# Optimization experiments

Measured on AMD Instinct MI355X. Metric: run time of the kernel, lower is better.

## Reference

```python
import jax, jax.numpy as jnp
import numpy as np

N, T, F_IN, HEADS, FILT = 50000, 12, 128, 4, 32
D = HEADS * FILT  # 128
E = 800000
NEG_SLOPE = 0.2  # PyG GATConv default leaky_relu slope


def setup_inputs() -> dict:
    key = jax.random.key(0)
    ks = jax.random.split(key, 10)
    s = lambda k, shape, fan: (jax.random.normal(k, shape, jnp.float32) / np.float32(np.sqrt(fan)))
    x_sequence = jax.random.normal(ks[0], (N, T, F_IN), dtype=jnp.float32)
    edge_index_sequence = jax.random.randint(ks[1], (T, 2, E), 0, N, dtype=jnp.int32)
    W_gat = s(ks[2], (F_IN, D), F_IN)          # GATConv lin weight
    a_src = s(ks[3], (HEADS, FILT), FILT)      # att_src
    a_dst = s(ks[4], (HEADS, FILT), FILT)      # att_dst
    b_gat = jnp.zeros((D,), jnp.float32)
    W_ih = s(ks[5], (3 * D, D), D)             # GRU weight_ih_l0 (r,z,n)
    W_hh = s(ks[6], (3 * D, D), D)             # GRU weight_hh_l0
    b_ih = jnp.zeros((3 * D,), jnp.float32)
    b_hh = jnp.zeros((3 * D,), jnp.float32)
    W_lin = s(ks[7], (1, D), D)
    b_lin = jnp.zeros((1,), jnp.float32)
    return dict(x_sequence=x_sequence, edge_index_sequence=edge_index_sequence,
                W_gat=W_gat, a_src=a_src, a_dst=a_dst, b_gat=b_gat,
                W_ih=W_ih, W_hh=W_hh, b_ih=b_ih, b_hh=b_hh,
                W_lin=W_lin, b_lin=b_lin)


def _gat_t(x_t, src, dst, W_gat, a_src, a_dst, b_gat):
    # x_t: [N, F_IN], src/dst: [E+N] (self-loops appended, PyG default)
    h = (x_t @ W_gat).reshape(N, HEADS, FILT)          # [N, H, C]
    al_src = jnp.sum(h * a_src, axis=-1)               # [N, H]
    al_dst = jnp.sum(h * a_dst, axis=-1)               # [N, H]
    e = jax.nn.leaky_relu(al_src[src] + al_dst[dst], NEG_SLOPE)  # [Etot, H]
    m = jax.ops.segment_max(e, dst, num_segments=N)    # softmax over incoming edges per dst node
    e = jnp.exp(e - m[dst])
    denom = jax.ops.segment_sum(e, dst, num_segments=N)
    alpha = e / (denom[dst] + 1e-16)                   # [Etot, H]
    msg = h[src] * alpha[:, :, None]                   # [Etot, H, C]
    out = jax.ops.segment_sum(msg, dst, num_segments=N)
    return out.reshape(N, D) + b_gat                   # concat heads + bias


def reference(x_sequence, edge_index_sequence, W_gat, a_src, a_dst, b_gat,
              W_ih, W_hh, b_ih, b_hh, W_lin, b_lin):
    x_tnf = jnp.transpose(x_sequence, (1, 0, 2))       # [T, N, F_IN]
    loops = jnp.arange(N, dtype=edge_index_sequence.dtype)
    src = jnp.concatenate([edge_index_sequence[:, 0, :], jnp.broadcast_to(loops, (T, N))], axis=1)
    dst = jnp.concatenate([edge_index_sequence[:, 1, :], jnp.broadcast_to(loops, (T, N))], axis=1)
    gat = jax.vmap(lambda x, s, d: _gat_t(x, s, d, W_gat, a_src, a_dst, b_gat))
    g = jax.nn.relu(gat(x_tnf, src, dst))              # [T, N, D]

    def gru_step(h, x):  # torch GRU gate order: r, z, n
        gi = x @ W_ih.T + b_ih
        gh = h @ W_hh.T + b_hh
        i_r, i_z, i_n = jnp.split(gi, 3, axis=-1)
        h_r, h_z, h_n = jnp.split(gh, 3, axis=-1)
        r = jax.nn.sigmoid(i_r + h_r)
        z = jax.nn.sigmoid(i_z + h_z)
        n = jnp.tanh(i_n + r * h_n)
        return (1.0 - z) * n + z * h, None

    h0 = jnp.zeros((N, D), x_sequence.dtype)
    h_last, _ = jax.lax.scan(gru_step, h0, g)          # only last timestep output is used
    return (h_last @ W_lin.T + b_lin)[:, 0]            # [N]
```

## Files before the change

kernel.cpp:

```cpp
#include <hip/hip_runtime.h>
#include <cstddef>

#define NN 50000
#define TT 12
#define FIN 128
#define DD 128
#define HH 4
#define EE 800000
#define MTOT (NN * TT)
#define NEG 0.2f

#define BSH 6
#define NB 782
#define CAPB 1536
#define BMAX CAPB
#define EPB2 8192
#define FB2 98
#define GGRID (TT * NB)
#define GPX (GGRID / 8)

typedef __attribute__((ext_vector_type(8))) short bf16x8;
typedef __attribute__((ext_vector_type(4))) float f32x4;

__device__ __forceinline__ ushort f2b(float x) {
    unsigned int u = __builtin_bit_cast(unsigned int, x);
    unsigned int r = (u + 0x7FFFu + ((u >> 16) & 1u)) >> 16;
    return (ushort)r;
}
__device__ __forceinline__ float b2f(ushort u) {
    unsigned int v = ((unsigned int)u) << 16;
    return __builtin_bit_cast(float, v);
}

__global__ __launch_bounds__(256) void prep_wg_kernel(
    const float* __restrict__ Wg, ushort* __restrict__ Wgh, ushort* __restrict__ Wgl)
{
    int idx = blockIdx.x * 256 + threadIdx.x;
    int fi = idx >> 9, rem = idx & 511;
    int l = rem >> 3, j = rem & 7;
    int kb = fi >> 3, cf = fi & 7;
    int k = kb * 32 + (l >> 4) * 8 + j;
    int col = cf * 16 + (l & 15);
    float v = Wg[(size_t)k * DD + col];
    ushort hi = f2b(v);
    Wgh[idx] = hi;
    Wgl[idx] = f2b(v - b2f(hi));
}

__global__ __launch_bounds__(256) void gemm_all_kernel(
    const float* __restrict__ x, const ushort* __restrict__ Wgh, const ushort* __restrict__ Wgl,
    const float* __restrict__ a_src, const float* __restrict__ a_dst,
    ushort* __restrict__ hbf, float* __restrict__ alsrc, float* __restrict__ aldst)
{
    __shared__ ushort sAh[64 * 128];
    const int tid = threadIdx.x;
    const int w = tid >> 6, l = tid & 63;
    const int m0 = blockIdx.x * 64;

    #pragma unroll
    for (int i = 0; i < 8; i++) {
        int fl = tid + 256 * i;
        int row = fl >> 5, q = fl & 31;
        float4 v = *(const float4*)&x[(size_t)(m0 + row) * FIN + q * 4];
        ushort hi[4] = {f2b(v.x), f2b(v.y), f2b(v.z), f2b(v.w)};
        int byteoff = row * 256 + ((q * 8) ^ ((row & 7) << 4));
        *(uint2*)((char*)sAh + byteoff) = *(uint2*)hi;
    }
    __syncthreads();

    f32x4 acc[4][2];
    #pragma unroll
    for (int i = 0; i < 4; i++)
        #pragma unroll
        for (int s = 0; s < 2; s++) acc[i][s] = (f32x4){0.f, 0.f, 0.f, 0.f};

    const bf16x8* Bh = (const bf16x8*)Wgh;
    const bf16x8* Bl = (const bf16x8*)Wgl;
    #pragma unroll
    for (int kb = 0; kb < 4; kb++) {
        bf16x8 ah[4];
        #pragma unroll
        for (int i = 0; i < 4; i++) {
            int rl = i * 16 + (l & 15);
            int byteoff = rl * 256 + (((kb * 64) + ((l >> 4) * 16)) ^ ((rl & 7) << 4));
            ah[i] = *(const bf16x8*)((const char*)sAh + byteoff);
        }
        bf16x8 bh[2], bl[2];
        #pragma unroll
        for (int s = 0; s < 2; s++) {
            int fi = kb * 8 + 2 * w + s;
            bh[s] = Bh[(size_t)fi * 64 + l];
            bl[s] = Bl[(size_t)fi * 64 + l];
        }
        #pragma unroll
        for (int i = 0; i < 4; i++)
            #pragma unroll
            for (int s = 0; s < 2; s++) {
                acc[i][s] = __builtin_amdgcn_mfma_f32_16x16x32_bf16(ah[i], bh[s], acc[i][s], 0, 0, 0);
                acc[i][s] = __builtin_amdgcn_mfma_f32_16x16x32_bf16(ah[i], bl[s], acc[i][s], 0, 0, 0);
            }
    }

    #pragma unroll
    for (int i = 0; i < 4; i++)
        #pragma unroll
        for (int s = 0; s < 2; s++) {
            int jj = (2 * w + s) * 16 + (l & 15);
            #pragma unroll
            for (int r = 0; r < 4; r++) {
                int m = m0 + i * 16 + (l >> 4) * 4 + r;
                int n = m / TT;
                int t = m - n * TT;
                hbf[((size_t)t * NN + n) * DD + jj] = f2b(acc[i][s][r]);
            }
        }

    const float as0 = a_src[w * 32 + (l & 15)];
    const float as1 = a_src[w * 32 + 16 + (l & 15)];
    const float ad0 = a_dst[w * 32 + (l & 15)];
    const float ad1 = a_dst[w * 32 + 16 + (l & 15)];
    #pragma unroll
    for (int i = 0; i < 4; i++) {
        #pragma unroll
        for (int r = 0; r < 4; r++) {
            float p1 = acc[i][0][r] * as0 + acc[i][1][r] * as1;
            float p2 = acc[i][0][r] * ad0 + acc[i][1][r] * ad1;
            #pragma unroll
            for (int mk = 1; mk < 16; mk <<= 1) {
                p1 += __shfl_xor(p1, mk);
                p2 += __shfl_xor(p2, mk);
            }
            if ((l & 15) == 0) {
                int m = m0 + i * 16 + (l >> 4) * 4 + r;
                int n = m / TT;
                int t = m - n * TT;
                size_t base = ((size_t)t * NN + n) * 4 + w;
                alsrc[base] = p1;
                aldst[base] = p2;
            }
        }
    }
}

__global__ __launch_bounds__(256) void init_cur_kernel(int* __restrict__ cur)
{
    int i = blockIdx.x * 256 + threadIdx.x;
    if (i < TT * NB) cur[i] = i * CAPB;
}

__global__ __launch_bounds__(512) void fill2_kernel(
    const int* __restrict__ ei, int* __restrict__ cur, uint* __restrict__ bbuf)
{
    __shared__ int hcnt[NB];
    __shared__ int hbase[NB];
    const int t = blockIdx.x / FB2;
    const int blk = blockIdx.x - t * FB2;
    const int tid = threadIdx.x;
    const int* srcp = ei + (size_t)t * 2 * EE;
    const int* dstp = srcp + EE;

    for (int b = tid; b < NB; b += 512) hcnt[b] = 0;
    __syncthreads();

    const int ebase = blk * EPB2;
    uint vals[16];
    #pragma unroll
    for (int k = 0; k < 16; k++) {
        int e = ebase + k * 512 + tid;
        uint v = 0xffffffffu;
        if (e < EE) {
            int s = srcp[e];
            int d = dstp[e];
            v = ((uint)d << 16) | (uint)s;
            atomicAdd(&hcnt[d >> BSH], 1);
        }
        vals[k] = v;
    }
    __syncthreads();
    for (int b = tid; b < NB; b += 512) {
        int c = hcnt[b];
        if (c > 0) hbase[b] = atomicAdd(&cur[t * NB + b], c);
        hcnt[b] = 0;
    }
    __syncthreads();
    #pragma unroll
    for (int k = 0; k < 16; k++) {
        uint v = vals[k];
        if (v != 0xffffffffu) {
            int b = v >> 22;
            int r = atomicAdd(&hcnt[b], 1);
            bbuf[hbase[b] + r] = v;
        }
    }
}

__global__ __launch_bounds__(512) void gather_all_kernel(
    const int* __restrict__ cur, const uint* __restrict__ bbuf,
    const float* __restrict__ alsrc_a, const float* __restrict__ aldst_a,
    const uint* __restrict__ hbf32_a, const float* __restrict__ bgat,
    uint* __restrict__ Ag_a)
{
    __shared__ uint ent[BMAX];
    __shared__ ushort ssrc[BMAX];
    __shared__ int h64[64];
    __shared__ int p64[65];
    __shared__ int cur64[64];
    const int bid = blockIdx.x;
    const int swz = (bid & 7) * GPX + (bid >> 3);
    const int t = swz / NB;
    const int bkt = swz - t * NB;
    const int ci = t * NB + bkt;
    const int tid = threadIdx.x;
    const int dbase = bkt << BSH;

    const float* alsrc = alsrc_a + (size_t)t * NN * HH;
    const float* aldst = aldst_a + (size_t)t * NN * HH;
    const uint* hbf32 = hbf32_a + (size_t)t * NN * 64;
    uint* Ag = Ag_a + (size_t)t * NN * 64;

    const int lo0 = ci * CAPB;
    int cnt = cur[ci] - lo0;
    if (cnt > BMAX) cnt = BMAX;

    if (tid < 64) h64[tid] = 0;
    __syncthreads();
    for (int i = tid; i < cnt; i += 512) {
        uint e = bbuf[lo0 + i];
        ent[i] = e;
        atomicAdd(&h64[(e >> 16) & 63], 1);
    }
    __syncthreads();
    if (tid < 64) {
        int v = h64[tid];
        #pragma unroll
        for (int off = 1; off < 64; off <<= 1) {
            int u = __shfl_up(v, off);
            if (tid >= off) v += u;
        }
        p64[tid + 1] = v;
        if (tid == 0) p64[0] = 0;
        cur64[tid] = v - h64[tid];
    }
    __syncthreads();
    for (int i = tid; i < cnt; i += 512) {
        uint e = ent[i];
        int pos = atomicAdd(&cur64[(e >> 16) & 63], 1);
        ssrc[pos] = (ushort)(e & 0xffffu);
    }
    __syncthreads();

    const int w = tid >> 6, lane = tid & 63, hd = lane >> 4;
    const float bg0 = bgat[2 * lane], bg1 = bgat[2 * lane + 1];
    for (int q = 0; q < 8; q++) {
        int nd = w * 8 + q;
        int d = dbase + nd;
        if (d >= NN) break;
        float adh = aldst[(size_t)d * 4 + hd];
        float a = alsrc[(size_t)d * 4 + hd] + adh;
        a = fmaxf(a, NEG * a);
        float wt = __expf(a);
        float den = wt;
        uint hw = hbf32[(size_t)d * 64 + lane];
        float acc0 = __builtin_bit_cast(float, hw << 16) * wt;
        float acc1 = __builtin_bit_cast(float, hw & 0xffff0000u) * wt;
        const int e1 = p64[nd + 1];
        #pragma unroll 2
        for (int e = p64[nd]; e < e1; e++) {
            int s = ssrc[e];
            float aa = alsrc[(size_t)s * 4 + hd] + adh;
            aa = fmaxf(aa, NEG * aa);
            float wgt = __expf(aa);
            uint hh = hbf32[(size_t)s * 64 + lane];
            acc0 += __builtin_bit_cast(float, hh << 16) * wgt;
            acc1 += __builtin_bit_cast(float, hh & 0xffff0000u) * wgt;
            den += wgt;
        }
        float invd = 1.f / (den + 1e-16f);
        float g0 = fmaxf(acc0 * invd + bg0, 0.f);
        float g1 = fmaxf(acc1 * invd + bg1, 0.f);
        Ag[(size_t)d * 64 + lane] = (uint)f2b(g0) | ((uint)f2b(g1) << 16);
    }
}

__global__ __launch_bounds__(256) void prep_b_kernel(
    const float* __restrict__ Wih, const float* __restrict__ Whh, ushort* __restrict__ Bswz)
{
    int idx = blockIdx.x * 256 + threadIdx.x;
    int fi = idx >> 9;
    int rem = idx & 511;
    int l = rem >> 3, j = rem & 7;
    int kb = fi >> 5, c = fi & 31;
    int g = c >> 3, cf = c & 7;
    int k = kb * 32 + (l >> 4) * 8 + j;
    int jj = cf * 16 + (l & 15);
    float v;
    if (g == 0)      v = (k < 128) ? Wih[(size_t)jj * DD + k]         : Whh[(size_t)jj * DD + k - 128];
    else if (g == 1) v = (k < 128) ? Wih[(size_t)(128 + jj) * DD + k] : Whh[(size_t)(128 + jj) * DD + k - 128];
    else if (g == 2) v = (k < 128) ? Wih[(size_t)(256 + jj) * DD + k] : 0.f;
    else             v = (k < 128) ? 0.f : Whh[(size_t)(256 + jj) * DD + k - 128];
    Bswz[idx] = f2b(v);
}

__global__ __launch_bounds__(256, 2) void gru_mfma_kernel(
    const uint* __restrict__ Agp, const ushort* __restrict__ Bswz,
    float* __restrict__ hstate, const float* __restrict__ bih, const float* __restrict__ bhh,
    const float* __restrict__ wl, const float* __restrict__ bl,
    float* __restrict__ out, int last)
{
    __shared__ ushort sA[64 * 256];
    __shared__ float outacc[64];
    const int tid = threadIdx.x;
    const int w = tid >> 6, l = tid & 63;
    const int n0 = blockIdx.x * 64;

    if (tid < 64) outacc[tid] = 0.f;
    #pragma unroll
    for (int i = 0; i < 4; i++) {
        int flat = tid + 256 * i;
        int row = flat >> 4, gc = flat & 15;
        int n = n0 + row;
        uint4 vg = make_uint4(0u, 0u, 0u, 0u);
        ushort hv[8] = {0, 0, 0, 0, 0, 0, 0, 0};
        if (n < NN) {
            vg = *(const uint4*)&Agp[(size_t)n * 64 + gc * 4];
            float4 ha = *(const float4*)&hstate[(size_t)n * DD + gc * 8];
            float4 hb = *(const float4*)&hstate[(size_t)n * DD + gc * 8 + 4];
            hv[0] = f2b(ha.x); hv[1] = f2b(ha.y); hv[2] = f2b(ha.z); hv[3] = f2b(ha.w);
            hv[4] = f2b(hb.x); hv[5] = f2b(hb.y); hv[6] = f2b(hb.z); hv[7] = f2b(hb.w);
        }
        int sw = (row & 7) << 4;
        *(uint4*)((char*)sA + row * 512 + ((gc * 16) ^ sw)) = vg;
        *(uint4*)((char*)sA + row * 512 + ((256 + gc * 16) ^ sw)) = *(uint4*)hv;
    }
    __syncthreads();

    f32x4 acc[4][4][2];
    #pragma unroll
    for (int i = 0; i < 4; i++)
        #pragma unroll
        for (int g = 0; g < 4; g++)
            #pragma unroll
            for (int s = 0; s < 2; s++)
                acc[i][g][s] = (f32x4){0.f, 0.f, 0.f, 0.f};

    const bf16x8* Bf = (const bf16x8*)Bswz;
    #pragma unroll
    for (int kb = 0; kb < 8; kb++) {
        bf16x8 a[4];
        #pragma unroll
        for (int i = 0; i < 4; i++) {
            int rl = i * 16 + (l & 15);
            int byteoff = rl * 512 + (((kb * 64) + ((l >> 4) * 16)) ^ ((rl & 7) << 4));
            a[i] = *(const bf16x8*)((const char*)sA + byteoff);
        }
        bf16x8 b[4][2];
        #pragma unroll
        for (int g = 0; g < 4; g++)
            #pragma unroll
            for (int s = 0; s < 2; s++)
                b[g][s] = Bf[(size_t)(kb * 32 + g * 8 + 2 * w + s) * 64 + l];
        #pragma unroll
        for (int i = 0; i < 4; i++)
            #pragma unroll
            for (int g = 0; g < 4; g++)
                #pragma unroll
                for (int s = 0; s < 2; s++)
                    acc[i][g][s] = __builtin_amdgcn_mfma_f32_16x16x32_bf16(
                        a[i], b[g][s], acc[i][g][s], 0, 0, 0);
    }

    #pragma unroll
    for (int s = 0; s < 2; s++) {
        int jj = (2 * w + s) * 16 + (l & 15);
        float br  = bih[jj] + bhh[jj];
        float bz  = bih[128 + jj] + bhh[128 + jj];
        float bin = bih[256 + jj];
        float bhn = bhh[256 + jj];
        float wlc = wl[jj];
        #pragma unroll
        for (int i = 0; i < 4; i++) {
            #pragma unroll
            for (int r = 0; r < 4; r++) {
                int row = i * 16 + (l >> 4) * 4 + r;
                int n = n0 + row;
                if (n >= NN) continue;
                float rp = acc[i][0][s][r] + br;
                float zp = acc[i][1][s][r] + bz;
                float rg = 1.f / (1.f + __expf(-rp));
                float zg = 1.f / (1.f + __expf(-zp));
                float nv = tanhf(acc[i][2][s][r] + bin + rg * (acc[i][3][s][r] + bhn));
                float hold = hstate[(size_t)n * DD + jj];
                float hnew = (1.f - zg) * nv + zg * hold;
                if (!last) hstate[(size_t)n * DD + jj] = hnew;
                else atomicAdd(&outacc[row], hnew * wlc);
            }
        }
    }
    if (last) {
        __syncthreads();
        int n = n0 + tid;
        if (tid < 64 && n < NN) out[n] = outacc[tid] + bl[0];
    }
}

extern "C" void kernel_launch(void* const* d_in, const int* in_sizes, int n_in,
                              void* d_out, int out_size, void* d_ws, size_t ws_size,
                              hipStream_t stream)
{
    const float* x     = (const float*)d_in[0];
    const int*   ei    = (const int*)d_in[1];
    const float* Wg    = (const float*)d_in[2];
    const float* a_src = (const float*)d_in[3];
    const float* a_dst = (const float*)d_in[4];
    const float* b_gat = (const float*)d_in[5];
    const float* Wih   = (const float*)d_in[6];
    const float* Whh   = (const float*)d_in[7];
    const float* bih   = (const float*)d_in[8];
    const float* bhh   = (const float*)d_in[9];
    const float* Wl    = (const float*)d_in[10];
    const float* bl    = (const float*)d_in[11];
    float* out = (float*)d_out;

    char* ws = (char*)d_ws;
    float* hstate  = (float*)ws;                                  ws += (size_t)NN * DD * 4;
    float* alsrc   = (float*)ws;                                  ws += (size_t)MTOT * HH * 4;
    float* aldst   = (float*)ws;                                  ws += (size_t)MTOT * HH * 4;
    uint* Agall    = (uint*)ws;                                   ws += (size_t)MTOT * 64 * 4;
    ushort* Bswz   = (ushort*)ws;                                 ws += 131072 * 2;
    ushort* Wgh    = (ushort*)ws;                                 ws += 16384 * 2;
    ushort* Wgl    = (ushort*)ws;                                 ws += 16384 * 2;
    ushort* hbf    = (ushort*)ws;                                 ws += (size_t)MTOT * DD * 2;
    int* cur       = (int*)ws;                                    ws += (size_t)TT * NB * 4;
    uint* bbuf     = (uint*)ws;                                   ws += (size_t)TT * NB * CAPB * 4;

    hipMemsetAsync(hstate, 0, (size_t)NN * DD * sizeof(float), stream);

    init_cur_kernel<<<(TT * NB + 255) / 256, 256, 0, stream>>>(cur);
    prep_b_kernel<<<512, 256, 0, stream>>>(Wih, Whh, Bswz);
    prep_wg_kernel<<<64, 256, 0, stream>>>(Wg, Wgh, Wgl);

    gemm_all_kernel<<<MTOT / 64, 256, 0, stream>>>(x, Wgh, Wgl, a_src, a_dst, hbf, alsrc, aldst);

    fill2_kernel<<<TT * FB2, 512, 0, stream>>>(ei, cur, bbuf);
    gather_all_kernel<<<GGRID, 512, 0, stream>>>(
        cur, bbuf, alsrc, aldst, (const uint*)hbf, b_gat, Agall);

    for (int t = 0; t < TT; t++) {
        gru_mfma_kernel<<<(NN + 63) / 64, 256, 0, stream>>>(
            Agall + (size_t)t * NN * 64, Bswz, hstate, bih, bhh, Wl, bl, out, t == TT - 1);
    }
}
```

Baseline: 1.179 ms.

## Fuse three GRU timesteps per launch, keep bf16 hidden state in LDS

The GRU kernel now runs three timesteps per launch, so there are four launches instead of twelve. The hidden state stays in shared memory as bf16 between steps and is written to global memory (as bf16 instead of fp32) only after the third step. This cuts global hidden-state traffic and launch count. It also raises the gather loop unroll from 2 to 4. The hidden state is now carried in bf16 across steps, which adds some rounding error compared with the fp32 hstate before.

```diff
diff --git a/kernel.cpp b/kernel.cpp
--- a/kernel.cpp
+++ b/kernel.cpp
@@ -264,7 +264,7 @@
         float acc0 = __builtin_bit_cast(float, hw << 16) * wt;
         float acc1 = __builtin_bit_cast(float, hw & 0xffff0000u) * wt;
         const int e1 = p64[nd + 1];
-        #pragma unroll 2
+        #pragma unroll 4
         for (int e = p64[nd]; e < e1; e++) {
             int s = ssrc[e];
             float aa = alsrc[(size_t)s * 4 + hd] + adh;
@@ -302,10 +302,11 @@
 }
 
 __global__ __launch_bounds__(256, 2) void gru_mfma_kernel(
-    const uint* __restrict__ Agp, const ushort* __restrict__ Bswz,
-    float* __restrict__ hstate, const float* __restrict__ bih, const float* __restrict__ bhh,
+    const uint* __restrict__ Agall, int tbase,
+    uint* __restrict__ Ah, const ushort* __restrict__ Bswz,
+    const float* __restrict__ bih, const float* __restrict__ bhh,
     const float* __restrict__ wl, const float* __restrict__ bl,
-    float* __restrict__ out, int last)
+    float* __restrict__ out)
 {
     __shared__ ushort sA[64 * 256];
     __shared__ float outacc[64];
@@ -319,84 +320,110 @@
         int flat = tid + 256 * i;
         int row = flat >> 4, gc = flat & 15;
         int n = n0 + row;
-        uint4 vg = make_uint4(0u, 0u, 0u, 0u);
-        ushort hv[8] = {0, 0, 0, 0, 0, 0, 0, 0};
-        if (n < NN) {
-            vg = *(const uint4*)&Agp[(size_t)n * 64 + gc * 4];
-            float4 ha = *(const float4*)&hstate[(size_t)n * DD + gc * 8];
-            float4 hb = *(const float4*)&hstate[(size_t)n * DD + gc * 8 + 4];
-            hv[0] = f2b(ha.x); hv[1] = f2b(ha.y); hv[2] = f2b(ha.z); hv[3] = f2b(ha.w);
-            hv[4] = f2b(hb.x); hv[5] = f2b(hb.y); hv[6] = f2b(hb.z); hv[7] = f2b(hb.w);
-        }
+        uint4 vh = make_uint4(0u, 0u, 0u, 0u);
+        if (n < NN) vh = *(const uint4*)&Ah[(size_t)n * 64 + gc * 4];
         int sw = (row & 7) << 4;
-        *(uint4*)((char*)sA + row * 512 + ((gc * 16) ^ sw)) = vg;
-        *(uint4*)((char*)sA + row * 512 + ((256 + gc * 16) ^ sw)) = *(uint4*)hv;
-    }
-    __syncthreads();
-
-    f32x4 acc[4][4][2];
-    #pragma unroll
-    for (int i = 0; i < 4; i++)
-        #pragma unroll
-        for (int g = 0; g < 4; g++)
-            #pragma unroll
-            for (int s = 0; s < 2; s++)
-                acc[i][g][s] = (f32x4){0.f, 0.f, 0.f, 0.f};
+        *(uint4*)((char*)sA + row * 512 + ((256 + gc * 16) ^ sw)) = vh;
+    }
+
+    const int jjA[2] = { (2 * w) * 16 + (l & 15), (2 * w + 1) * 16 + (l & 15) };
+    float brc[2], bzc[2], binc[2], bhnc[2], wlc[2];
+    #pragma unroll
+    for (int s = 0; s < 2; s++) {
+        brc[s]  = bih[jjA[s]] + bhh[jjA[s]];
+        bzc[s]  = bih[128 + jjA[s]] + bhh[128 + jjA[s]];
+        binc[s] = bih[256 + jjA[s]];
+        bhnc[s] = bhh[256 + jjA[s]];
+        wlc[s]  = wl[jjA[s]];
+    }
 
     const bf16x8* Bf = (const bf16x8*)Bswz;
-    #pragma unroll
-    for (int kb = 0; kb < 8; kb++) {
-        bf16x8 a[4];
+
+    #pragma unroll 1
+    for (int tt = 0; tt < 3; tt++) {
+        const int t = tbase + tt;
+        const uint* Agp = Agall + (size_t)t * NN * 64;
         #pragma unroll
         for (int i = 0; i < 4; i++) {
-            int rl = i * 16 + (l & 15);
-            int byteoff = rl * 512 + (((kb * 64) + ((l >> 4) * 16)) ^ ((rl & 7) << 4));
-            a[i] = *(const bf16x8*)((const char*)sA + byteoff);
-        }
-        bf16x8 b[4][2];
-        #pragma unroll
-        for (int g = 0; g < 4; g++)
-            #pragma unroll
-            for (int s = 0; s < 2; s++)
-                b[g][s] = Bf[(size_t)(kb * 32 + g * 8 + 2 * w + s) * 64 + l];
+            int flat = tid + 256 * i;
+            int row = flat >> 4, gc = flat & 15;
+            int n = n0 + row;
+            uint4 vg = make_uint4(0u, 0u, 0u, 0u);
+            if (n < NN) vg = *(const uint4*)&Agp[(size_t)n * 64 + gc * 4];
+            int sw = (row & 7) << 4;
+            *(uint4*)((char*)sA + row * 512 + ((gc * 16) ^ sw)) = vg;
+        }
+        __syncthreads();
+
+        f32x4 acc[4][4][2];
         #pragma unroll
         for (int i = 0; i < 4; i++)
             #pragma unroll
             for (int g = 0; g < 4; g++)
                 #pragma unroll
                 for (int s = 0; s < 2; s++)
-                    acc[i][g][s] = __builtin_amdgcn_mfma_f32_16x16x32_bf16(
-                        a[i], b[g][s], acc[i][g][s], 0, 0, 0);
-    }
-
-    #pragma unroll
-    for (int s = 0; s < 2; s++) {
-        int jj = (2 * w + s) * 16 + (l & 15);
-        float br  = bih[jj] + bhh[jj];
-        float bz  = bih[128 + jj] + bhh[128 + jj];
-        float bin = bih[256 + jj];
-        float bhn = bhh[256 + jj];
-        float wlc = wl[jj];
-        #pragma unroll
-        for (int i = 0; i < 4; i++) {
-            #pragma unroll
-            for (int r = 0; r < 4; r++) {
-                int row = i * 16 + (l >> 4) * 4 + r;
-                int n = n0 + row;
-                if (n >= NN) continue;
-                float rp = acc[i][0][s][r] + br;
-                float zp = acc[i][1][s][r] + bz;
-                float rg = 1.f / (1.f + __expf(-rp));
-                float zg = 1.f / (1.f + __expf(-zp));
-                float nv = tanhf(acc[i][2][s][r] + bin + rg * (acc[i][3][s][r] + bhn));
-                float hold = hstate[(size_t)n * DD + jj];
-                float hnew = (1.f - zg) * nv + zg * hold;
-                if (!last) hstate[(size_t)n * DD + jj] = hnew;
-                else atomicAdd(&outacc[row], hnew * wlc);
-            }
-        }
-    }
-    if (last) {
+                    acc[i][g][s] = (f32x4){0.f, 0.f, 0.f, 0.f};
+
+        #pragma unroll
+        for (int kb = 0; kb < 8; kb++) {
+            bf16x8 a[4];
+            #pragma unroll
+            for (int i = 0; i < 4; i++) {
+                int rl = i * 16 + (l & 15);
+                int byteoff = rl * 512 + (((kb * 64) + ((l >> 4) * 16)) ^ ((rl & 7) << 4));
+                a[i] = *(const bf16x8*)((const char*)sA + byteoff);
+            }
+            bf16x8 b[4][2];
+            #pragma unroll
+            for (int g = 0; g < 4; g++)
+                #pragma unroll
+                for (int s = 0; s < 2; s++)
+                    b[g][s] = Bf[(size_t)(kb * 32 + g * 8 + 2 * w + s) * 64 + l];
+            #pragma unroll
+            for (int i = 0; i < 4; i++)
+                #pragma unroll
+                for (int g = 0; g < 4; g++)
+                    #pragma unroll
+                    for (int s = 0; s < 2; s++)
+                        acc[i][g][s] = __builtin_amdgcn_mfma_f32_16x16x32_bf16(
+                            a[i], b[g][s], acc[i][g][s], 0, 0, 0);
+        }
+        __syncthreads();
+
+        const bool lastT = (t == TT - 1);
+        #pragma unroll
+        for (int s = 0; s < 2; s++) {
+            const int jj = jjA[s];
+            const int hc = 16 + (jj >> 3);
+            const int hb = (jj & 7) * 2;
+            #pragma unroll
+            for (int i = 0; i < 4; i++) {
+                #pragma unroll
+                for (int r = 0; r < 4; r++) {
+                    int row = i * 16 + (l >> 4) * 4 + r;
+                    int n = n0 + row;
+                    if (n >= NN) continue;
+                    int hoff = row * 512 + ((hc * 16) ^ ((row & 7) << 4)) + hb;
+                    float hold = b2f(*(const ushort*)((const char*)sA + hoff));
+                    float rp = acc[i][0][s][r] + brc[s];
+                    float zp = acc[i][1][s][r] + bzc[s];
+                    float rg = 1.f / (1.f + __expf(-rp));
+                    float zg = 1.f / (1.f + __expf(-zp));
+                    float nv = tanhf(acc[i][2][s][r] + binc[s] + rg * (acc[i][3][s][r] + bhnc[s]));
+                    float hnew = (1.f - zg) * nv + zg * hold;
+                    if (lastT) {
+                        atomicAdd(&outacc[row], hnew * wlc[s]);
+                    } else {
+                        ushort hb16 = f2b(hnew);
+                        *(ushort*)((char*)sA + hoff) = hb16;
+                        if (tt == 2) ((ushort*)Ah)[(size_t)n * 128 + jj] = hb16;
+                    }
+                }
+            }
+        }
+    }
+
+    if (tbase + 2 == TT - 1) {
         __syncthreads();
         int n = n0 + tid;
         if (tid < 64 && n < NN) out[n] = outacc[tid] + bl[0];
@@ -422,10 +449,10 @@
     float* out = (float*)d_out;
 
     char* ws = (char*)d_ws;
-    float* hstate  = (float*)ws;                                  ws += (size_t)NN * DD * 4;
     float* alsrc   = (float*)ws;                                  ws += (size_t)MTOT * HH * 4;
     float* aldst   = (float*)ws;                                  ws += (size_t)MTOT * HH * 4;
     uint* Agall    = (uint*)ws;                                   ws += (size_t)MTOT * 64 * 4;
+    uint* Ah       = (uint*)ws;                                   ws += (size_t)NN * 64 * 4;
     ushort* Bswz   = (ushort*)ws;                                 ws += 131072 * 2;
     ushort* Wgh    = (ushort*)ws;                                 ws += 16384 * 2;
     ushort* Wgl    = (ushort*)ws;                                 ws += 16384 * 2;
@@ -433,7 +460,7 @@
     int* cur       = (int*)ws;                                    ws += (size_t)TT * NB * 4;
     uint* bbuf     = (uint*)ws;                                   ws += (size_t)TT * NB * CAPB * 4;
 
-    hipMemsetAsync(hstate, 0, (size_t)NN * DD * sizeof(float), stream);
+    hipMemsetAsync(Ah, 0, (size_t)NN * 64 * sizeof(uint), stream);
 
     init_cur_kernel<<<(TT * NB + 255) / 256, 256, 0, stream>>>(cur);
     prep_b_kernel<<<512, 256, 0, stream>>>(Wih, Whh, Bswz);
@@ -445,8 +472,8 @@
     gather_all_kernel<<<GGRID, 512, 0, stream>>>(
         cur, bbuf, alsrc, aldst, (const uint*)hbf, b_gat, Agall);
 
-    for (int t = 0; t < TT; t++) {
+    for (int tb = 0; tb < TT; tb += 3) {
         gru_mfma_kernel<<<(NN + 63) / 64, 256, 0, stream>>>(
-            Agall + (size_t)t * NN * 64, Bswz, hstate, bih, bhh, Wl, bl, out, t == TT - 1);
-    }
-}
+            Agall, tb, Ah, Bswz, bih, bhh, Wl, bl, out);
+    }
+}
```

Result: slower. 1.799 ms (+52.6%).
